# Kernel tuning notes

Hardware: AMD Instinct MI355X
Metric: run time of the kernel (lower is better)

The kernel has to match this reference:

```python
import jax, jax.numpy as jnp
import numpy as np

A = 4096       # padded atoms
M = 64         # max neighbors
DIM_Q = 64     # descriptor dim
H = 128        # hidden neurons
NUM_TYPES = 8
BOX_L = 30.0   # cubic cell length (Angstrom-ish)


def setup_inputs() -> dict:
    key = jax.random.key(0)
    ks = jax.random.split(key, 10)
    descriptors = jax.random.normal(ks[0], (A, DIM_Q), dtype=jnp.float32)
    gradients = jax.random.normal(ks[1], (A, M, 3, DIM_Q), dtype=jnp.float32) * 0.1
    grad_index = jax.random.randint(ks[2], (A, M), 0, A)
    positions = jax.random.uniform(ks[3], (A, 3), dtype=jnp.float32) * BOX_L
    Z = jax.random.randint(ks[4], (A,), 0, NUM_TYPES)
    box = BOX_L * jnp.eye(3, dtype=jnp.float32)
    atom_mask = jnp.ones((A,), dtype=jnp.float32)
    neighbor_mask = (jax.random.uniform(ks[5], (A, M)) < 0.9).astype(jnp.float32)
    # learned parameters (glorot-ish scale)
    W0 = jax.random.normal(ks[6], (NUM_TYPES, DIM_Q, H), dtype=jnp.float32) * (2.0 / (DIM_Q + H)) ** 0.5
    b0 = jnp.zeros((NUM_TYPES, H), dtype=jnp.float32)
    W1 = jax.random.normal(ks[7], (NUM_TYPES, H), dtype=jnp.float32) * (2.0 / (H + 1)) ** 0.5
    b1 = jnp.zeros((), dtype=jnp.float32)
    return {"descriptors": descriptors, "gradients": gradients, "grad_index": grad_index,
            "positions": positions, "Z": Z, "box": box, "atom_mask": atom_mask,
            "neighbor_mask": neighbor_mask, "W0": W0, "b0": b0, "W1": W1, "b1": b1}


def _neighbor_displacements(positions, box, grad_index):
    # minimum-image displacements r_j - r_i for each padded neighbor slot
    dr = positions[grad_index] - positions[:, None, :]          # [A, M, 3]
    inv_box = jnp.linalg.inv(box)
    frac = dr @ inv_box
    frac = frac - jnp.round(frac)
    dr = frac @ box
    rij = jnp.sqrt(jnp.sum(dr * dr, axis=-1))                   # [A, M] distances
    return dr, rij


def reference(descriptors, gradients, grad_index, positions, Z, box, atom_mask, neighbor_mask, W0, b0, W1, b1):
    # per-atom type-gathered weights (deterministic MoE routing by atom type)
    W0_t = W0[Z]                                                # [A, dim_q, H]
    b0_t = b0[Z]                                                # [A, H]
    W1_t = W1[Z]                                                # [A, H]
    # batched small MLP
    h = jnp.einsum('nd,ndh->nh', descriptors, W0_t) + b0_t
    h = jnp.tanh(h)
    h = h * atom_mask[:, None]                                  # [A, H]
    # chain-rule forces dU_i/dR_j
    dtanh = 1.0 - jnp.square(h)
    de_da = dtanh * W1_t                                        # [A, H]
    de_dq = jnp.einsum('nh,nqh->nq', de_da, W0_t)               # [A, dim_q]
    forces = jnp.einsum('nq,nmcq->nmc', de_dq, gradients)       # [A, M, 3]
    forces = forces * neighbor_mask[:, :, None]
    # dipole: -sum_ij |r_ij|^2 * forces
    _, rij = _neighbor_displacements(positions, box, grad_index)
    rij2 = jnp.square(rij) * neighbor_mask                      # [A, M]
    dipole = -jnp.sum(rij2[:, :, None] * forces, axis=(0, 1))   # [3]
    return dipole
```

## Files before the change

kernel.cpp:

```cpp
#include <hip/hip_runtime.h>

#define A_ 4096
#define M_ 64
#define Q_ 64
#define H_ 128

__global__ __launch_bounds__(256, 4) void tnep_fused(
    const float* __restrict__ desc,
    const float* __restrict__ grad,
    const int*   __restrict__ gidx,
    const float* __restrict__ pos,
    const int*   __restrict__ Zt,
    const float* __restrict__ box,
    const float* __restrict__ amask,
    const float* __restrict__ nmask,
    const float* __restrict__ W0,
    const float* __restrict__ b0,
    const float* __restrict__ W1,
    float* __restrict__ partials)
{
    __shared__ __align__(16) float desc_s[Q_];
    __shared__ __align__(16) float dedq_s[Q_];
    __shared__ float coef_s[M_];
    __shared__ float psumF[8 * 132];
    __shared__ __align__(16) float deda_s[H_];
    __shared__ float psumB[Q_ * 33];
    __shared__ float wred[3][4];

    const int n = blockIdx.x;
    const int t = threadIdx.x;

    const float4* gbase = (const float4*)(grad + (size_t)n * (M_ * 3 * Q_));
    float4 gpre[12];
    #pragma unroll
    for (int i = 0; i < 12; ++i) gpre[i] = gbase[i * 256 + t];
    __builtin_amdgcn_sched_barrier(0);

    const int z = Zt[n];

    const float4* W0z4 = (const float4*)(W0 + (size_t)z * (Q_ * H_));
    float4 w0r[8];
    #pragma unroll
    for (int k = 0; k < 8; ++k) w0r[k] = W0z4[t + 256 * k];
    __builtin_amdgcn_sched_barrier(0);

    if (t < 16) ((float4*)desc_s)[t] = ((const float4*)(desc + n * Q_))[t];

    if (t >= 64 && t < 128) {
        int m = t - 64;
        float b00 = box[0], b01 = box[1], b02 = box[2];
        float b10 = box[3], b11 = box[4], b12 = box[5];
        float b20 = box[6], b21 = box[7], b22 = box[8];
        float c00 =   b11 * b22 - b12 * b21;
        float c01 = -(b10 * b22 - b12 * b20);
        float c02 =   b10 * b21 - b11 * b20;
        float det = b00 * c00 + b01 * c01 + b02 * c02;
        float id  = 1.0f / det;
        float i00 = c00 * id;
        float i10 = c01 * id;
        float i20 = c02 * id;
        float i01 = -(b01 * b22 - b02 * b21) * id;
        float i11 =  (b00 * b22 - b02 * b20) * id;
        float i21 = -(b00 * b21 - b01 * b20) * id;
        float i02 =  (b01 * b12 - b02 * b11) * id;
        float i12 = -(b00 * b12 - b02 * b10) * id;
        float i22 =  (b00 * b11 - b01 * b10) * id;

        int j = gidx[n * M_ + m];
        float dx = pos[j * 3 + 0] - pos[n * 3 + 0];
        float dy = pos[j * 3 + 1] - pos[n * 3 + 1];
        float dz = pos[j * 3 + 2] - pos[n * 3 + 2];
        float fx = dx * i00 + dy * i10 + dz * i20;
        float fy = dx * i01 + dy * i11 + dz * i21;
        float fz = dx * i02 + dy * i12 + dz * i22;
        fx -= rintf(fx); fy -= rintf(fy); fz -= rintf(fz);
        float rx = fx * b00 + fy * b10 + fz * b20;
        float ry = fx * b01 + fy * b11 + fz * b21;
        float rz = fx * b02 + fy * b12 + fz * b22;
        float nm = nmask[n * M_ + m];
        coef_s[m] = -((rx * rx + ry * ry + rz * rz) * nm) * nm;
    }
    __syncthreads();

    {
        const int g = t >> 5;
        const int hbase = (t & 31) * 4;
        float fx = 0.f, fy = 0.f, fz = 0.f, fw = 0.f;
        #pragma unroll
        for (int k = 0; k < 8; ++k) {
            float d = desc_s[g + 8 * k];
            float4 w = w0r[k];
            fx += d * w.x; fy += d * w.y; fz += d * w.z; fw += d * w.w;
        }
        psumF[g * 132 + hbase + 0] = fx;
        psumF[g * 132 + hbase + 1] = fy;
        psumF[g * 132 + hbase + 2] = fz;
        psumF[g * 132 + hbase + 3] = fw;
    }
    __syncthreads();

    if (t < H_) {
        float pre = b0[z * H_ + t];
        #pragma unroll
        for (int g = 0; g < 8; ++g) pre += psumF[g * 132 + t];
        float am = amask[n];
        float hv = tanhf(pre) * am;
        deda_s[t] = (1.0f - hv * hv) * W1[z * H_ + t];
    }
    __syncthreads();

    {
        float4 dd = ((const float4*)deda_s)[t & 31];
        #pragma unroll
        for (int k = 0; k < 8; ++k) {
            int q = (t >> 5) + 8 * k;
            float4 w = w0r[k];
            psumB[q * 33 + (t & 31)] =
                w.x * dd.x + w.y * dd.y + w.z * dd.z + w.w * dd.w;
        }
    }
    __syncthreads();

    if (t < Q_) {
        float s = 0.0f;
        #pragma unroll
        for (int v = 0; v < 32; ++v) s += psumB[t * 33 + v];
        dedq_s[t] = s;
    }
    __syncthreads();

    float a0 = 0.f, a1 = 0.f, a2 = 0.f;
    const float4* dq4 = (const float4*)dedq_s;
    #pragma unroll
    for (int i = 0; i < 12; ++i) {
        int idx = i * 256 + t;
        int m   = idx / 48;
        int rc  = idx - m * 48;
        int c   = rc >> 4;
        int q4  = rc & 15;
        float4 g = gpre[i];
        float4 d = dq4[q4];
        float  p = (g.x * d.x + g.y * d.y + g.z * d.z + g.w * d.w) * coef_s[m];
        a0 += (c == 0) ? p : 0.0f;
        a1 += (c == 1) ? p : 0.0f;
        a2 += (c == 2) ? p : 0.0f;
    }

    #pragma unroll
    for (int off = 32; off > 0; off >>= 1) {
        a0 += __shfl_down(a0, off);
        a1 += __shfl_down(a1, off);
        a2 += __shfl_down(a2, off);
    }
    if ((t & 63) == 0) {
        int w = t >> 6;
        wred[0][w] = a0; wred[1][w] = a1; wred[2][w] = a2;
    }
    __syncthreads();

    if (t == 0) {
        partials[n]          = (wred[0][0] + wred[0][1]) + (wred[0][2] + wred[0][3]);
        partials[A_ + n]     = (wred[1][0] + wred[1][1]) + (wred[1][2] + wred[1][3]);
        partials[2 * A_ + n] = (wred[2][0] + wred[2][1]) + (wred[2][2] + wred[2][3]);
    }
}

__global__ __launch_bounds__(1024) void tnep_reduce(
    const float* __restrict__ partials, float* __restrict__ out)
{
    __shared__ float sb0[1024], sb1[1024], sb2[1024];
    const int t = threadIdx.x;
    const float4* p4 = (const float4*)partials;
    float4 a = p4[t];
    float4 b = p4[1024 + t];
    float4 c = p4[2048 + t];
    sb0[t] = (a.x + a.y) + (a.z + a.w);
    sb1[t] = (b.x + b.y) + (b.z + b.w);
    sb2[t] = (c.x + c.y) + (c.z + c.w);
    __syncthreads();
    #pragma unroll
    for (int off = 512; off > 0; off >>= 1) {
        if (t < off) {
            sb0[t] += sb0[t + off];
            sb1[t] += sb1[t + off];
            sb2[t] += sb2[t + off];
        }
        __syncthreads();
    }
    if (t == 0) { out[0] = sb0[0]; out[1] = sb1[0]; out[2] = sb2[0]; }
}

extern "C" void kernel_launch(void* const* d_in, const int* in_sizes, int n_in,
                              void* d_out, int out_size, void* d_ws, size_t ws_size,
                              hipStream_t stream) {
    const float* desc  = (const float*)d_in[0];
    const float* grad  = (const float*)d_in[1];
    const int*   gidx  = (const int*)  d_in[2];
    const float* pos   = (const float*)d_in[3];
    const int*   Zt    = (const int*)  d_in[4];
    const float* box   = (const float*)d_in[5];
    const float* amask = (const float*)d_in[6];
    const float* nmask = (const float*)d_in[7];
    const float* W0    = (const float*)d_in[8];
    const float* b0    = (const float*)d_in[9];
    const float* W1    = (const float*)d_in[10];

    float* partials = (float*)d_ws;
    float* out      = (float*)d_out;

    tnep_fused<<<A_, 256, 0, stream>>>(desc, grad, gidx, pos, Zt, box,
                                       amask, nmask, W0, b0, W1, partials);
    tnep_reduce<<<1, 1024, 0, stream>>>(partials, out);
}
```

Before: 41.36 us.

## Split fused kernel into MLP stage and gradient streaming stage

```diff
diff --git a/kernel.cpp b/kernel.cpp
--- a/kernel.cpp
+++ b/kernel.cpp
@@ -5,9 +5,9 @@
 #define Q_ 64
 #define H_ 128
 
-__global__ __launch_bounds__(256, 4) void tnep_fused(
+
+__global__ __launch_bounds__(256) void tnep_mlp(
     const float* __restrict__ desc,
-    const float* __restrict__ grad,
     const int*   __restrict__ gidx,
     const float* __restrict__ pos,
     const int*   __restrict__ Zt,
@@ -17,32 +17,22 @@
     const float* __restrict__ W0,
     const float* __restrict__ b0,
     const float* __restrict__ W1,
-    float* __restrict__ partials)
+    float* __restrict__ dedq_g,
+    float* __restrict__ coef_g)
 {
     __shared__ __align__(16) float desc_s[Q_];
-    __shared__ __align__(16) float dedq_s[Q_];
-    __shared__ float coef_s[M_];
     __shared__ float psumF[8 * 132];
     __shared__ __align__(16) float deda_s[H_];
     __shared__ float psumB[Q_ * 33];
-    __shared__ float wred[3][4];
 
     const int n = blockIdx.x;
     const int t = threadIdx.x;
-
-    const float4* gbase = (const float4*)(grad + (size_t)n * (M_ * 3 * Q_));
-    float4 gpre[12];
-    #pragma unroll
-    for (int i = 0; i < 12; ++i) gpre[i] = gbase[i * 256 + t];
-    __builtin_amdgcn_sched_barrier(0);
-
     const int z = Zt[n];
 
     const float4* W0z4 = (const float4*)(W0 + (size_t)z * (Q_ * H_));
     float4 w0r[8];
     #pragma unroll
     for (int k = 0; k < 8; ++k) w0r[k] = W0z4[t + 256 * k];
-    __builtin_amdgcn_sched_barrier(0);
 
     if (t < 16) ((float4*)desc_s)[t] = ((const float4*)(desc + n * Q_))[t];
 
@@ -78,7 +68,7 @@
         float ry = fx * b01 + fy * b11 + fz * b21;
         float rz = fx * b02 + fy * b12 + fz * b22;
         float nm = nmask[n * M_ + m];
-        coef_s[m] = -((rx * rx + ry * ry + rz * rz) * nm) * nm;
+        coef_g[n * M_ + m] = -((rx * rx + ry * ry + rz * rz) * nm) * nm;
     }
     __syncthreads();
 
@@ -125,21 +115,43 @@
         float s = 0.0f;
         #pragma unroll
         for (int v = 0; v < 32; ++v) s += psumB[t * 33 + v];
-        dedq_s[t] = s;
-    }
+        dedq_g[n * Q_ + t] = s;
+    }
+}
+
+__global__ __launch_bounds__(256, 6) void tnep_stream(
+    const float* __restrict__ grad,
+    const float* __restrict__ dedq_g,
+    const float* __restrict__ coef_g,
+    float* __restrict__ partials)
+{
+    __shared__ __align__(16) float4 dedq_s[16];
+    __shared__ __align__(16) float  coef_s[M_];
+    __shared__ float wred[3][4];
+
+    const int n = blockIdx.x;
+    const int t = threadIdx.x;
+
+    const float4* gbase = (const float4*)(grad + (size_t)n * (M_ * 3 * Q_));
+    float4 gpre[12];
+    #pragma unroll
+    for (int i = 0; i < 12; ++i) gpre[i] = gbase[i * 256 + t];
+    __builtin_amdgcn_sched_barrier(0);
+
+    if (t < 16)       dedq_s[t] = ((const float4*)(dedq_g + n * Q_))[t];
+    else if (t < 32)  ((float4*)coef_s)[t - 16] =
+                          ((const float4*)(coef_g + n * M_))[t - 16];
     __syncthreads();
 
     float a0 = 0.f, a1 = 0.f, a2 = 0.f;
-    const float4* dq4 = (const float4*)dedq_s;
+    const float4 d = dedq_s[t & 15];
     #pragma unroll
     for (int i = 0; i < 12; ++i) {
         int idx = i * 256 + t;
         int m   = idx / 48;
         int rc  = idx - m * 48;
         int c   = rc >> 4;
-        int q4  = rc & 15;
         float4 g = gpre[i];
-        float4 d = dq4[q4];
         float  p = (g.x * d.x + g.y * d.y + g.z * d.z + g.w * d.w) * coef_s[m];
         a0 += (c == 0) ? p : 0.0f;
         a1 += (c == 1) ? p : 0.0f;
@@ -205,10 +217,14 @@
     const float* b0    = (const float*)d_in[9];
     const float* W1    = (const float*)d_in[10];
 
-    float* partials = (float*)d_ws;
+    float* ws       = (float*)d_ws;
+    float* dedq_g   = ws;
+    float* coef_g   = ws + A_ * Q_;
+    float* partials = ws + 2 * A_ * Q_;
     float* out      = (float*)d_out;
 
-    tnep_fused<<<A_, 256, 0, stream>>>(desc, grad, gidx, pos, Zt, box,
-                                       amask, nmask, W0, b0, W1, partials);
+    tnep_mlp<<<A_, 256, 0, stream>>>(desc, gidx, pos, Zt, box, amask, nmask,
+                                     W0, b0, W1, dedq_g, coef_g);
+    tnep_stream<<<A_, 256, 0, stream>>>(grad, dedq_g, coef_g, partials);
     tnep_reduce<<<1, 1024, 0, stream>>>(partials, out);
 }
```

Measured after the change: 48.23 us. +16.6%, slower.
